# Performance work log

Measured on AMD Instinct MI355X. Metric: run time of the kernel, lower is better.

## Reference

```python
import jax, jax.numpy as jnp
import numpy as np

K = 3          # kernel_size
EPS = 1e-12    # epsilon from l2_normal and abs-clamp


def setup_inputs() -> dict:
    key = jax.random.key(0)
    k1, k2 = jax.random.split(key)
    B, H, W, C, F = 8, 224, 224, 32, 32
    image = jax.random.normal(k1, (B, H, W, C), dtype=jnp.float32)
    # glorot-uniform-ish weight, shape (1, C*K*K, filters)
    fan = C * K * K + F
    lim = np.sqrt(6.0 / fan).astype(np.float32)
    w = jax.random.uniform(k2, (1, C * K * K, F), dtype=jnp.float32, minval=-lim, maxval=lim)
    p = jnp.full((F,), 100.0 ** 0.5, dtype=jnp.float32)   # p init = sqrt(100)
    q = jnp.full((1,), 10.0 ** 0.5, dtype=jnp.float32)    # q init = sqrt(10)
    return {"image": image, "w": w, "p": p, "q": q}


def reference(image, w, p, q):
    # CosSim2D, kernel_size=3, stride=1, padding='same', non-depthwise.
    B, H, W, C = image.shape
    pad = K // 2
    padded = jnp.pad(image, ((0, 0), (pad, pad), (pad, pad), (0, 0)))
    # im2col: kernel-position-major, channel-minor -> matches tf.stack(axis=3) + reshape
    patches = jnp.stack(
        [padded[:, dy:dy + H, dx:dx + W, :] for dy in range(K) for dx in range(K)],
        axis=3,
    )  # (B, H, W, K*K, C)
    x = patches.reshape(B, H * W, K * K * C)
    q_term = jnp.square(q) / 10.0                       # scalar (broadcast)
    x_norm = jnp.sqrt(jnp.maximum(jnp.sum(x * x, axis=2, keepdims=True), EPS)) + q_term
    w_norm = jnp.sqrt(jnp.maximum(jnp.sum(w * w, axis=1, keepdims=True), EPS)) + q_term
    sim = jnp.matmul(x / x_norm, (w / w_norm)[0])       # (B, H*W, filters)
    out = jnp.sign(sim) * jnp.power(jnp.abs(sim) + EPS, jnp.square(p) / 100.0)
    return out.reshape(B, H, W, -1)
```

## Files before the change

### kernel.cpp

```cpp
#include <hip/hip_runtime.h>
#include <hip/hip_bf16.h>


#define H_ 224
#define W_ 224
#define C_ 32
#define F_ 32

#define NSTEP 18
#define HROWS 10
#define HCOLS 34

typedef __bf16 bf16_t;
typedef bf16_t bf16x8 __attribute__((ext_vector_type(8)));
typedef float f32x16 __attribute__((ext_vector_type(16)));

#define WFRAG_BYTES (NSTEP * 64 * 8 * 2)

__global__ __launch_bounds__(256) void cos2d_prep(
    const float* __restrict__ w, const float* __restrict__ p,
    const float* __restrict__ q, bf16_t* __restrict__ wfrag,
    float* __restrict__ winv, float* __restrict__ ef) {
  __shared__ float part[8][32];
  const int tid = threadIdx.x;
  const int f = tid & 31, kg = tid >> 5;
  float s = 0.f;
#pragma unroll
  for (int i = 0; i < 36; ++i) {
    const float v = w[(kg + 8 * i) * F_ + f];
    s += v * v;
  }
  part[kg][f] = s;
  __syncthreads();
  if (tid < 32) {
    float t = 0.f;
#pragma unroll
    for (int g = 0; g < 8; ++g) t += part[g][tid];
    const float qt = q[0] * q[0] * 0.1f;
    winv[tid] = 1.f / (sqrtf(fmaxf(t, 1e-12f)) + qt);
    ef[tid] = p[tid] * p[tid] * 0.01f;
  }
  for (int t = tid; t < NSTEP * 64; t += 256) {
    const int s2 = t >> 6, l = t & 63;
    const int ff = l & 31;
    union { bf16_t v[8]; uint4 u; } tv;
#pragma unroll
    for (int e = 0; e < 8; ++e) {
      const int kk = s2 * 16 + ((l >> 5) << 3) + e;
      tv.v[e] = (bf16_t)w[kk * F_ + ff];
    }
    *(uint4*)(wfrag + (size_t)t * 8) = tv.u;
  }
}

__global__ __launch_bounds__(256, 4) void cos2d_main(
    const float* __restrict__ img, const bf16_t* __restrict__ wfrag,
    const float* __restrict__ winv, const float* __restrict__ ef,
    const float* __restrict__ q, float* __restrict__ out) {
  __shared__ bf16_t xt[HROWS][HCOLS][40];
  __shared__ float ssum[HROWS][HCOLS];

  const int tid = threadIdx.x;
  const int lane = tid & 63;
  const int wv = tid >> 6;
  const int lp = lane & 31;

  const int bid = blockIdx.x;
  const int tw = bid % 7;
  const int th = (bid / 7) % 28;
  const int b  = bid / 196;
  const int h0 = th * 8, w0 = tw * 32;

  const float qt = q[0] * q[0] * 0.1f;
  const float efv = ef[lp];
  const float wnv = winv[lp];

  bf16x8 bfrag[NSTEP];
  const bf16x8* wf4 = (const bf16x8*)wfrag;
#pragma unroll
  for (int s2 = 0; s2 < NSTEP; ++s2) bfrag[s2] = wf4[s2 * 64 + lane];

  for (int idx = tid; idx < HROWS * HCOLS * 8; idx += 256) {
    const int p = idx >> 3, sub = idx & 7;
    const int rr = p / HCOLS, cc = p - rr * HCOLS;
    const int hh = h0 - 1 + rr, wc = w0 - 1 + cc;
    float4 v = make_float4(0.f, 0.f, 0.f, 0.f);
    if ((unsigned)hh < H_ && (unsigned)wc < W_)
      v = *(const float4*)(img + ((size_t)(b * H_ + hh) * W_ + wc) * C_ + sub * 4);
    float s = v.x * v.x + v.y * v.y + v.z * v.z + v.w * v.w;
    s += __shfl_xor(s, 1);
    s += __shfl_xor(s, 2);
    s += __shfl_xor(s, 4);
    union { bf16_t h[4]; uint2 u; } pk;
    pk.h[0] = (bf16_t)v.x; pk.h[1] = (bf16_t)v.y;
    pk.h[2] = (bf16_t)v.z; pk.h[3] = (bf16_t)v.w;
    *(uint2*)&xt[rr][cc][sub * 4] = pk.u;
    if (sub == 0) ssum[rr][cc] = s;
  }
  __syncthreads();

  const int mr0 = wv * 2;

  float xinv[2];
#pragma unroll
  for (int t = 0; t < 2; ++t) {
    const int mr = mr0 + t;
    const float xn2 = ssum[mr + 0][lp] + ssum[mr + 0][lp + 1] + ssum[mr + 0][lp + 2]
                    + ssum[mr + 1][lp] + ssum[mr + 1][lp + 1] + ssum[mr + 1][lp + 2]
                    + ssum[mr + 2][lp] + ssum[mr + 2][lp + 1] + ssum[mr + 2][lp + 2];
    xinv[t] = 1.f / (sqrtf(fmaxf(xn2, 1e-12f)) + qt);
  }

  f32x16 acc0, acc1;
#pragma unroll
  for (int i = 0; i < 16; ++i) { acc0[i] = 0.f; acc1[i] = 0.f; }

#pragma unroll
  for (int s2 = 0; s2 < NSTEP; ++s2) {
    const int pos = s2 >> 1;
    const int dy = pos / 3, dx = pos - dy * 3;
    const int chof = (s2 & 1) * 16 + ((lane >> 5) << 3);
    const bf16x8 a0 = *(const bf16x8*)&xt[mr0 + 0 + dy][lp + dx][chof];
    const bf16x8 a1 = *(const bf16x8*)&xt[mr0 + 1 + dy][lp + dx][chof];
    acc0 = __builtin_amdgcn_mfma_f32_32x32x16_bf16(a0, bfrag[s2], acc0, 0, 0, 0);
    acc1 = __builtin_amdgcn_mfma_f32_32x32x16_bf16(a1, bfrag[s2], acc1, 0, 0, 0);
  }

#pragma unroll
  for (int t = 0; t < 2; ++t) {
    const f32x16& acc = t ? acc1 : acc0;
    const int obase = (b * H_ + h0 + mr0 + t) * W_ + w0;
#pragma unroll
    for (int jj = 0; jj < 16; ++jj) {
      const int row = (jj & 3) + 8 * (jj >> 2) + 4 * (lane >> 5);
      const float xi = __shfl(xinv[t], row);
      const float sim = acc[jj] * xi * wnv;
      const float ps = fabsf(sim) + 1e-12f;
      float r = exp2f(efv * __log2f(ps));
      r = copysignf(r, sim);
      out[(size_t)(obase + row) * F_ + lp] = r;
    }
  }
}

extern "C" void kernel_launch(void* const* d_in, const int* in_sizes, int n_in,
                              void* d_out, int out_size, void* d_ws, size_t ws_size,
                              hipStream_t stream) {
  const float* img = (const float*)d_in[0];
  const float* w   = (const float*)d_in[1];
  const float* p   = (const float*)d_in[2];
  const float* q   = (const float*)d_in[3];

  bf16_t* wfrag = (bf16_t*)d_ws;
  float*  winv  = (float*)((char*)d_ws + WFRAG_BYTES);
  float*  ef    = winv + 64;

  cos2d_prep<<<1, 256, 0, stream>>>(w, p, q, wfrag, winv, ef);
  cos2d_main<<<1568, 256, 0, stream>>>(img, wfrag, winv, ef, q, (float*)d_out);
}
```

Measured before the change: 37.77 us.

## Make main kernel persistent with register-prefetched double-buffered LDS tiles

Converts the main kernel from one block per tile into a persistent grid of 512 blocks that loop over tiles. Each iteration issues the global loads for the next tile into registers before running the MFMA compute on the current tile, then commits them into a second LDS buffer. Weight fragments are now reloaded from global memory at every step instead of being held in registers, and occupancy is reduced to 2 blocks per SM. The prep kernel is also spread over 6 blocks. In exchange there is more register pressure (11 float4 prefetch slots), double the LDS use, and tail imbalance because 1568 tiles do not divide evenly over 512 blocks.

```diff
diff --git a/kernel.cpp b/kernel.cpp
--- a/kernel.cpp
+++ b/kernel.cpp
@@ -10,6 +10,10 @@
 #define NSTEP 18
 #define HROWS 10
 #define HCOLS 34
+#define NSLOT 11
+#define SLOTS (HROWS * HCOLS * 8)
+#define GRIDSZ 512
+#define NTILES 1568
 
 typedef __bf16 bf16_t;
 typedef bf16_t bf16x8 __attribute__((ext_vector_type(8)));
@@ -21,125 +25,163 @@
     const float* __restrict__ w, const float* __restrict__ p,
     const float* __restrict__ q, bf16_t* __restrict__ wfrag,
     float* __restrict__ winv, float* __restrict__ ef) {
-  __shared__ float part[8][32];
   const int tid = threadIdx.x;
-  const int f = tid & 31, kg = tid >> 5;
-  float s = 0.f;
-#pragma unroll
-  for (int i = 0; i < 36; ++i) {
-    const float v = w[(kg + 8 * i) * F_ + f];
-    s += v * v;
-  }
-  part[kg][f] = s;
-  __syncthreads();
-  if (tid < 32) {
-    float t = 0.f;
-#pragma unroll
-    for (int g = 0; g < 8; ++g) t += part[g][tid];
-    const float qt = q[0] * q[0] * 0.1f;
-    winv[tid] = 1.f / (sqrtf(fmaxf(t, 1e-12f)) + qt);
-    ef[tid] = p[tid] * p[tid] * 0.01f;
-  }
-  for (int t = tid; t < NSTEP * 64; t += 256) {
-    const int s2 = t >> 6, l = t & 63;
-    const int ff = l & 31;
-    union { bf16_t v[8]; uint4 u; } tv;
-#pragma unroll
-    for (int e = 0; e < 8; ++e) {
-      const int kk = s2 * 16 + ((l >> 5) << 3) + e;
-      tv.v[e] = (bf16_t)w[kk * F_ + ff];
-    }
-    *(uint4*)(wfrag + (size_t)t * 8) = tv.u;
+  if (blockIdx.x == 0) {
+    __shared__ float part[8][32];
+    const int f = tid & 31, kg = tid >> 5;
+    float s = 0.f;
+#pragma unroll
+    for (int i = 0; i < 36; ++i) {
+      const float v = w[(kg + 8 * i) * F_ + f];
+      s += v * v;
+    }
+    part[kg][f] = s;
+    __syncthreads();
+    if (tid < 32) {
+      float t = 0.f;
+#pragma unroll
+      for (int g = 0; g < 8; ++g) t += part[g][tid];
+      const float qt = q[0] * q[0] * 0.1f;
+      winv[tid] = 1.f / (sqrtf(fmaxf(t, 1e-12f)) + qt);
+      ef[tid] = p[tid] * p[tid] * 0.01f;
+    }
+  } else {
+    const int t = (blockIdx.x - 1) * 256 + tid;
+    if (t < NSTEP * 64) {
+      const int s2 = t >> 6, l = t & 63;
+      const int ff = l & 31;
+      union { bf16_t v[8]; uint4 u; } tv;
+#pragma unroll
+      for (int e = 0; e < 8; ++e) {
+        const int kk = s2 * 16 + ((l >> 5) << 3) + e;
+        tv.v[e] = (bf16_t)w[kk * F_ + ff];
+      }
+      *(uint4*)(wfrag + (size_t)t * 8) = tv.u;
+    }
   }
 }
 
-__global__ __launch_bounds__(256, 4) void cos2d_main(
+__global__ __launch_bounds__(256, 2) void cos2d_main(
     const float* __restrict__ img, const bf16_t* __restrict__ wfrag,
     const float* __restrict__ winv, const float* __restrict__ ef,
     const float* __restrict__ q, float* __restrict__ out) {
-  __shared__ bf16_t xt[HROWS][HCOLS][40];
-  __shared__ float ssum[HROWS][HCOLS];
+  __shared__ bf16_t xt[2][HROWS][HCOLS][40];
+  __shared__ float ssum[2][HROWS][HCOLS];
 
   const int tid = threadIdx.x;
   const int lane = tid & 63;
   const int wv = tid >> 6;
   const int lp = lane & 31;
 
-  const int bid = blockIdx.x;
-  const int tw = bid % 7;
-  const int th = (bid / 7) % 28;
-  const int b  = bid / 196;
-  const int h0 = th * 8, w0 = tw * 32;
-
   const float qt = q[0] * q[0] * 0.1f;
   const float efv = ef[lp];
   const float wnv = winv[lp];
 
-  bf16x8 bfrag[NSTEP];
-  const bf16x8* wf4 = (const bf16x8*)wfrag;
-#pragma unroll
-  for (int s2 = 0; s2 < NSTEP; ++s2) bfrag[s2] = wf4[s2 * 64 + lane];
-
-  for (int idx = tid; idx < HROWS * HCOLS * 8; idx += 256) {
-    const int p = idx >> 3, sub = idx & 7;
-    const int rr = p / HCOLS, cc = p - rr * HCOLS;
-    const int hh = h0 - 1 + rr, wc = w0 - 1 + cc;
-    float4 v = make_float4(0.f, 0.f, 0.f, 0.f);
-    if ((unsigned)hh < H_ && (unsigned)wc < W_)
-      v = *(const float4*)(img + ((size_t)(b * H_ + hh) * W_ + wc) * C_ + sub * 4);
-    float s = v.x * v.x + v.y * v.y + v.z * v.z + v.w * v.w;
-    s += __shfl_xor(s, 1);
-    s += __shfl_xor(s, 2);
-    s += __shfl_xor(s, 4);
-    union { bf16_t h[4]; uint2 u; } pk;
-    pk.h[0] = (bf16_t)v.x; pk.h[1] = (bf16_t)v.y;
-    pk.h[2] = (bf16_t)v.z; pk.h[3] = (bf16_t)v.w;
-    *(uint2*)&xt[rr][cc][sub * 4] = pk.u;
-    if (sub == 0) ssum[rr][cc] = s;
-  }
+  float4 sv[NSLOT];
+
+  auto issue = [&](int tile) {
+    const int tw = tile % 7, th = (tile / 7) % 28, b = tile / 196;
+    const int h0 = th * 8, w0 = tw * 32;
+#pragma unroll
+    for (int k = 0; k < NSLOT; ++k) {
+      const int idx = tid + k * 256;
+      const int pp = idx >> 3, sub = idx & 7;
+      const int rr = pp / HCOLS, cc = pp - rr * HCOLS;
+      const int hh = h0 - 1 + rr, wc = w0 - 1 + cc;
+      float4 v = make_float4(0.f, 0.f, 0.f, 0.f);
+      if (idx < SLOTS && (unsigned)hh < H_ && (unsigned)wc < W_)
+        v = *(const float4*)(img + ((size_t)(b * H_ + hh) * W_ + wc) * C_ + sub * 4);
+      sv[k] = v;
+    }
+  };
+
+  auto commit = [&](int buf) {
+#pragma unroll
+    for (int k = 0; k < NSLOT; ++k) {
+      const int idx = tid + k * 256;
+      if (idx < SLOTS) {
+        const int pp = idx >> 3, sub = idx & 7;
+        const int rr = pp / HCOLS, cc = pp - rr * HCOLS;
+        const float4 v = sv[k];
+        float s = v.x * v.x + v.y * v.y + v.z * v.z + v.w * v.w;
+        s += __shfl_xor(s, 1);
+        s += __shfl_xor(s, 2);
+        s += __shfl_xor(s, 4);
+        union { bf16_t h[4]; uint2 u; } pk;
+        pk.h[0] = (bf16_t)v.x; pk.h[1] = (bf16_t)v.y;
+        pk.h[2] = (bf16_t)v.z; pk.h[3] = (bf16_t)v.w;
+        *(uint2*)&xt[buf][rr][cc][sub * 4] = pk.u;
+        if (sub == 0) ssum[buf][rr][cc] = s;
+      }
+    }
+  };
+
+  auto compute = [&](int tile, int buf) {
+    const int tw = tile % 7, th = (tile / 7) % 28, b = tile / 196;
+    const int h0 = th * 8, w0 = tw * 32;
+    const int mr0 = wv * 2;
+
+    float xinv[2];
+#pragma unroll
+    for (int t = 0; t < 2; ++t) {
+      const int mr = mr0 + t;
+      const float xn2 =
+          ssum[buf][mr + 0][lp] + ssum[buf][mr + 0][lp + 1] + ssum[buf][mr + 0][lp + 2] +
+          ssum[buf][mr + 1][lp] + ssum[buf][mr + 1][lp + 1] + ssum[buf][mr + 1][lp + 2] +
+          ssum[buf][mr + 2][lp] + ssum[buf][mr + 2][lp + 1] + ssum[buf][mr + 2][lp + 2];
+      xinv[t] = 1.f / (sqrtf(fmaxf(xn2, 1e-12f)) + qt);
+    }
+
+    f32x16 acc0, acc1;
+#pragma unroll
+    for (int i = 0; i < 16; ++i) { acc0[i] = 0.f; acc1[i] = 0.f; }
+
+    const bf16x8* wf4 = (const bf16x8*)wfrag;
+#pragma unroll
+    for (int s2 = 0; s2 < NSTEP; ++s2) {
+      const bf16x8 bf = wf4[s2 * 64 + lane];
+      const int pos = s2 >> 1;
+      const int dy = pos / 3, dx = pos - dy * 3;
+      const int chof = (s2 & 1) * 16 + ((lane >> 5) << 3);
+      const bf16x8 a0 = *(const bf16x8*)&xt[buf][mr0 + 0 + dy][lp + dx][chof];
+      const bf16x8 a1 = *(const bf16x8*)&xt[buf][mr0 + 1 + dy][lp + dx][chof];
+      acc0 = __builtin_amdgcn_mfma_f32_32x32x16_bf16(a0, bf, acc0, 0, 0, 0);
+      acc1 = __builtin_amdgcn_mfma_f32_32x32x16_bf16(a1, bf, acc1, 0, 0, 0);
+    }
+
+#pragma unroll
+    for (int t = 0; t < 2; ++t) {
+      const f32x16& acc = t ? acc1 : acc0;
+      const int obase = (b * H_ + h0 + mr0 + t) * W_ + w0;
+#pragma unroll
+      for (int jj = 0; jj < 16; ++jj) {
+        const int row = (jj & 3) + 8 * (jj >> 2) + 4 * (lane >> 5);
+        const float xi = __shfl(xinv[t], row);
+        const float sim = acc[jj] * xi * wnv;
+        const float ps = fabsf(sim) + 1e-12f;
+        float r = exp2f(efv * __log2f(ps));
+        r = copysignf(r, sim);
+        out[(size_t)(obase + row) * F_ + lp] = r;
+      }
+    }
+  };
+
+  int tile = blockIdx.x;
+  issue(tile);
+  commit(0);
   __syncthreads();
-
-  const int mr0 = wv * 2;
-
-  float xinv[2];
-#pragma unroll
-  for (int t = 0; t < 2; ++t) {
-    const int mr = mr0 + t;
-    const float xn2 = ssum[mr + 0][lp] + ssum[mr + 0][lp + 1] + ssum[mr + 0][lp + 2]
-                    + ssum[mr + 1][lp] + ssum[mr + 1][lp + 1] + ssum[mr + 1][lp + 2]
-                    + ssum[mr + 2][lp] + ssum[mr + 2][lp + 1] + ssum[mr + 2][lp + 2];
-    xinv[t] = 1.f / (sqrtf(fmaxf(xn2, 1e-12f)) + qt);
-  }
-
-  f32x16 acc0, acc1;
-#pragma unroll
-  for (int i = 0; i < 16; ++i) { acc0[i] = 0.f; acc1[i] = 0.f; }
-
-#pragma unroll
-  for (int s2 = 0; s2 < NSTEP; ++s2) {
-    const int pos = s2 >> 1;
-    const int dy = pos / 3, dx = pos - dy * 3;
-    const int chof = (s2 & 1) * 16 + ((lane >> 5) << 3);
-    const bf16x8 a0 = *(const bf16x8*)&xt[mr0 + 0 + dy][lp + dx][chof];
-    const bf16x8 a1 = *(const bf16x8*)&xt[mr0 + 1 + dy][lp + dx][chof];
-    acc0 = __builtin_amdgcn_mfma_f32_32x32x16_bf16(a0, bfrag[s2], acc0, 0, 0, 0);
-    acc1 = __builtin_amdgcn_mfma_f32_32x32x16_bf16(a1, bfrag[s2], acc1, 0, 0, 0);
-  }
-
-#pragma unroll
-  for (int t = 0; t < 2; ++t) {
-    const f32x16& acc = t ? acc1 : acc0;
-    const int obase = (b * H_ + h0 + mr0 + t) * W_ + w0;
-#pragma unroll
-    for (int jj = 0; jj < 16; ++jj) {
-      const int row = (jj & 3) + 8 * (jj >> 2) + 4 * (lane >> 5);
-      const float xi = __shfl(xinv[t], row);
-      const float sim = acc[jj] * xi * wnv;
-      const float ps = fabsf(sim) + 1e-12f;
-      float r = exp2f(efv * __log2f(ps));
-      r = copysignf(r, sim);
-      out[(size_t)(obase + row) * F_ + lp] = r;
-    }
+  int cur = 0;
+  for (;;) {
+    const int next = tile + GRIDSZ;
+    const bool have_next = next < NTILES;
+    if (have_next) issue(next);
+    compute(tile, cur);
+    if (!have_next) break;
+    __syncthreads();
+    commit(cur ^ 1);
+    __syncthreads();
+    cur ^= 1;
+    tile = next;
   }
 }
 
@@ -155,6 +197,6 @@
   float*  winv  = (float*)((char*)d_ws + WFRAG_BYTES);
   float*  ef    = winv + 64;
 
-  cos2d_prep<<<1, 256, 0, stream>>>(w, p, q, wfrag, winv, ef);
-  cos2d_main<<<1568, 256, 0, stream>>>(img, wfrag, winv, ef, q, (float*)d_out);
+  cos2d_prep<<<6, 256, 0, stream>>>(w, p, q, wfrag, winv, ef);
+  cos2d_main<<<GRIDSZ, 256, 0, stream>>>(img, wfrag, winv, ef, q, (float*)d_out);
 }
```

New measurement: 41.33 us. 1.09x slower.
